# Kernel optimization log

Measured on AMD Instinct MI355X. Metric: run time of the kernel, lower is better.

The kernel has to match this reference:

```python
import jax, jax.numpy as jnp
import numpy as np

K = 1e-3          # sigmoid temperature from MAPLoss(k=0.001): sigmoid(x) = 1/(1+exp(-x/K))
N, D = 512, 128   # batch of embeddings
NUM_CLASSES = 32
EPS = 1e-8


def setup_inputs() -> dict:
    key = jax.random.key(0)
    k1, k2 = jax.random.split(key)
    return {
        "input": jax.random.normal(k1, (N, D), dtype=jnp.float32),
        "target": jax.random.randint(k2, (N,), 0, NUM_CLASSES, dtype=jnp.int64),
    }


def _offdiag_cols(n):
    # cols[i, j] = j-th column index != i, in increasing order (matches
    # torch sm[~eye].view(n, n-1) row-major off-diagonal extraction)
    idx = jnp.arange(n - 1)[None, :]
    rows = jnp.arange(n)[:, None]
    return idx + (idx >= rows)  # [n, n-1] int


def reference(input, target):
    n = input.shape[0]
    # cosine similarity matrix
    norms = jnp.maximum(jnp.linalg.norm(input, axis=1, keepdims=True), EPS)
    xn = input / norms
    sm = xn @ xn.T  # [n, n]

    cols = _offdiag_cols(n)  # [n, n-1]
    ranking = jnp.take_along_axis(sm, cols, axis=1)  # [n, n-1]
    gt_full = (target[None, :] == target[:, None])    # [n, n] bool
    gt = jnp.take_along_axis(gt_full, cols, axis=1).astype(input.dtype)  # [n, n-1]

    # indicator[i, j, l] = sigmoid((r[i, l] - r[i, j]) / K)   -- O(n^3) cube
    indicator = jax.nn.sigmoid((ranking[:, None, :] - ranking[:, :, None]) / K)

    accumulated_gt = jnp.einsum('il,ijl->ij', gt, indicator)  # [n, n-1]
    denom = indicator.sum(-1) + 0.5                           # [n, n-1]
    prec = accumulated_gt / denom
    ap = jnp.sum(gt * prec, axis=1)    # [n]
    num_positives = gt.sum(-1)         # [n]

    valid = num_positives > 0
    ap_norm = jnp.where(valid, ap / jnp.where(valid, num_positives, 1.0), 0.0)
    n_valid = valid.sum().astype(input.dtype)
    return 1.0 - ap_norm.sum() / n_valid
```

## Files before the change

### kernel.cpp

```cpp
#include <hip/hip_runtime.h>

#define N 512
#define D 128
#define TS 32
#define RS_SCALE 1442.6950408889634f
#define W_INV (1.0f / 18.0f)
#define B_OFF 1530.0f
#define PADV -1600.0f
#define NB 172

static __device__ __forceinline__ float rcp_fast(float x) {
    return __builtin_amdgcn_rcpf(x);
}
static __device__ __forceinline__ float exp2_fast(float x) {
    return __builtin_amdgcn_exp2f(x);
}

__global__ __launch_bounds__(256) void map_sim_kernel(
    const float* __restrict__ x, float* __restrict__ rs,
    int* __restrict__ ticket)
{
    const int bi = blockIdx.x, bj = blockIdx.y, t = threadIdx.x;
    __shared__ float As[TS * D], Bs[TS * D];
    __shared__ float ssA[TS], ssB[TS];
    __shared__ float invA[TS], invB[TS];

    if (bi == 0 && bj == 0 && t == 0) *ticket = 0;

    const int lane = t & 63;
#pragma unroll
    for (int r = 0; r < 4; ++r) {
        int ch = t + 256 * r;
        int row = ch >> 5, c4 = ch & 31;
        int sw = (c4 ^ (row >> 1)) << 2;
        float4 va = *(const float4*)(x + (bi * TS + row) * D + c4 * 4);
        *(float4*)(As + row * D + sw) = va;
        float pa = va.x * va.x + va.y * va.y + va.z * va.z + va.w * va.w;
        float4 vb = *(const float4*)(x + (bj * TS + row) * D + c4 * 4);
        *(float4*)(Bs + row * D + sw) = vb;
        float pb = vb.x * vb.x + vb.y * vb.y + vb.z * vb.z + vb.w * vb.w;
#pragma unroll
        for (int off = 16; off; off >>= 1) {
            pa += __shfl_xor(pa, off);
            pb += __shfl_xor(pb, off);
        }
        if ((lane & 31) == 0) { ssA[row] = pa; ssB[row] = pb; }
    }
    __syncthreads();
    if (t < TS)          invA[t] = rcp_fast(fmaxf(sqrtf(ssA[t]), 1e-8f));
    else if (t < 2 * TS) invB[t - TS] = rcp_fast(fmaxf(sqrtf(ssB[t - TS]), 1e-8f));
    __syncthreads();

    const int tx = t & 15, ty = t >> 4;
    float acc00 = 0.f, acc01 = 0.f, acc10 = 0.f, acc11 = 0.f;
#pragma unroll 4
    for (int k4 = 0; k4 < D / 4; ++k4) {
        float4 a0 = *(const float4*)(As + (2 * ty) * D + ((k4 ^ ty) << 2));
        float4 a1 = *(const float4*)(As + (2 * ty + 1) * D + ((k4 ^ ty) << 2));
        float4 b0 = *(const float4*)(Bs + (2 * tx) * D + ((k4 ^ tx) << 2));
        float4 b1 = *(const float4*)(Bs + (2 * tx + 1) * D + ((k4 ^ tx) << 2));
        acc00 = fmaf(a0.x, b0.x, acc00); acc00 = fmaf(a0.y, b0.y, acc00);
        acc00 = fmaf(a0.z, b0.z, acc00); acc00 = fmaf(a0.w, b0.w, acc00);
        acc01 = fmaf(a0.x, b1.x, acc01); acc01 = fmaf(a0.y, b1.y, acc01);
        acc01 = fmaf(a0.z, b1.z, acc01); acc01 = fmaf(a0.w, b1.w, acc01);
        acc10 = fmaf(a1.x, b0.x, acc10); acc10 = fmaf(a1.y, b0.y, acc10);
        acc10 = fmaf(a1.z, b0.z, acc10); acc10 = fmaf(a1.w, b0.w, acc10);
        acc11 = fmaf(a1.x, b1.x, acc11); acc11 = fmaf(a1.y, b1.y, acc11);
        acc11 = fmaf(a1.z, b1.z, acc11); acc11 = fmaf(a1.w, b1.w, acc11);
    }

    const float sA0 = invA[2 * ty] * RS_SCALE;
    const float sA1 = invA[2 * ty + 1] * RS_SCALE;
    const float sB0 = invB[2 * tx], sB1 = invB[2 * tx + 1];
    const int gr = bi * TS + 2 * ty, gc = bj * TS + 2 * tx;
    *(float2*)(rs + gr * N + gc) =
        make_float2(acc00 * sA0 * sB0, acc01 * sA0 * sB1);
    *(float2*)(rs + (gr + 1) * N + gc) =
        make_float2(acc10 * sA1 * sB0, acc11 * sA1 * sB1);
}

__global__ __launch_bounds__(256) void map_ap_kernel(
    const float* __restrict__ rs, const int* __restrict__ tgt,
    float2* __restrict__ av, int* __restrict__ ticket,
    float* __restrict__ out)
{
    const int i = blockIdx.x, t = threadIdx.x;
    const int lane = t & 63;
    __shared__ int hist[256];
    __shared__ int offs[NB];
    __shared__ int wtot[4];
    __shared__ unsigned gbits[16];
    __shared__ __align__(16) float skey[N];
    __shared__ float red[8];
    __shared__ int amLast;

    const int ti = tgt[i];
    const float v0raw = rs[i * N + t];
    const float v1raw = rs[i * N + t + 256];
    const int tg0 = tgt[t], tg1 = tgt[t + 256];

    hist[t] = 0;
    if (t < NB) offs[t] = 0;
    if (t < 16) gbits[t] = 0u;

    float val[2]; int gti[2], q[2];
    val[0] = (t == i) ? PADV : v0raw;
    val[1] = (t + 256 == i) ? PADV : v1raw;
    gti[0] = (t != i && tg0 == ti) ? 1 : 0;
    gti[1] = (t + 256 != i && tg1 == ti) ? 1 : 0;
#pragma unroll
    for (int e = 0; e < 2; ++e) {
        int qq = (int)((val[e] + B_OFF) * W_INV);
        q[e] = max(0, min(NB - 1, qq));
    }
    __syncthreads();
    atomicAdd(&hist[q[0]], (1 << 10) | gti[0]);
    atomicAdd(&hist[q[1]], (1 << 10) | gti[1]);
    __syncthreads();

    int v = hist[t];
#pragma unroll
    for (int off = 1; off < 64; off <<= 1) {
        int u = __shfl_up(v, off);
        if (lane >= off) v += u;
    }
    if (lane == 63) wtot[t >> 6] = v;
    __syncthreads();
    {
        int w = t >> 6, add = 0;
        if (w > 0) add += wtot[0];
        if (w > 1) add += wtot[1];
        if (w > 2) add += wtot[2];
        hist[t] = v + add;
    }
    __syncthreads();

#pragma unroll
    for (int e = 0; e < 2; ++e) {
        int base = (q[e] > 0) ? (hist[q[e] - 1] >> 10) : 0;
        int pos = base + atomicAdd(&offs[q[e]], 1);
        skey[pos] = val[e];
        if (gti[e]) atomicOr(&gbits[pos >> 5], 1u << (pos & 31));
    }
    __syncthreads();

    const int totGt = hist[NB - 1] & 1023;
    const float4* sk4 = (const float4*)skey;

    float apAcc = 0.f, npAcc = 0.f;
#pragma unroll
    for (int ri = 0; ri < 2; ++ri) {
        const int p = t + 256 * ri;
        const float rj = skey[p];
        const float gtj = (float)((gbits[p >> 5] >> (p & 31)) & 1u);
        int qj = (int)((rj + B_OFF) * W_INV);
        qj = max(0, min(NB - 1, qj));
        const int qlo = __shfl(qj, 0);
        const int qhi = __shfl(qj, 63);
        const int lo = (qlo > 1) ? (hist[qlo - 2] >> 10) : 0;
        const int e1 = min(qhi + 1, NB - 1);
        const int hi = hist[e1] >> 10;

        float dsum = (float)(N - hi);
        float gsum = (float)(totGt - (hist[e1] & 1023));

        float d0 = 0.f, d1 = 0.f, d2 = 0.f, d3 = 0.f;
        float g0 = 0.f, g1 = 0.f, g2 = 0.f, g3 = 0.f;
        int k = lo & ~7;
        for (; k + 8 <= hi; k += 8) {
            float4 ka = sk4[k >> 2];
            float4 kb = sk4[(k >> 2) + 1];
            unsigned gw = (gbits[k >> 5] >> (k & 31)) & 0xffu;
            float s0 = rcp_fast(1.f + exp2_fast(rj - ka.x));
            float s1 = rcp_fast(1.f + exp2_fast(rj - ka.y));
            float s2 = rcp_fast(1.f + exp2_fast(rj - ka.z));
            float s3 = rcp_fast(1.f + exp2_fast(rj - ka.w));
            float s4 = rcp_fast(1.f + exp2_fast(rj - kb.x));
            float s5 = rcp_fast(1.f + exp2_fast(rj - kb.y));
            float s6 = rcp_fast(1.f + exp2_fast(rj - kb.z));
            float s7 = rcp_fast(1.f + exp2_fast(rj - kb.w));
            d0 += s0 + s4; d1 += s1 + s5; d2 += s2 + s6; d3 += s3 + s7;
            g0 += ((gw      ) & 1u) ? s0 : 0.f;
            g1 += ((gw >> 1u) & 1u) ? s1 : 0.f;
            g2 += ((gw >> 2u) & 1u) ? s2 : 0.f;
            g3 += ((gw >> 3u) & 1u) ? s3 : 0.f;
            g0 += ((gw >> 4u) & 1u) ? s4 : 0.f;
            g1 += ((gw >> 5u) & 1u) ? s5 : 0.f;
            g2 += ((gw >> 6u) & 1u) ? s6 : 0.f;
            g3 += ((gw >> 7u) & 1u) ? s7 : 0.f;
        }
        dsum += (d0 + d1) + (d2 + d3);
        gsum += (g0 + g1) + (g2 + g3);
        for (; k < hi; ++k) {
            float s = rcp_fast(1.f + exp2_fast(rj - skey[k]));
            dsum += s;
            gsum += ((gbits[k >> 5] >> (k & 31)) & 1u) ? s : 0.f;
        }

        apAcc += gtj * gsum * rcp_fast(dsum + 0.5f);
        npAcc += gtj;
    }

#pragma unroll
    for (int off = 32; off; off >>= 1) {
        apAcc += __shfl_down(apAcc, off);
        npAcc += __shfl_down(npAcc, off);
    }
    if (lane == 0) { red[(t >> 6) * 2] = apAcc; red[(t >> 6) * 2 + 1] = npAcc; }
    __syncthreads();
    if (t == 0) {
        float A = red[0] + red[2] + red[4] + red[6];
        float P = red[1] + red[3] + red[5] + red[7];
        av[i] = make_float2((P > 0.f) ? (A * rcp_fast(P)) : 0.f,
                            (P > 0.f) ? 1.f : 0.f);
        __threadfence();
        int old = atomicAdd(ticket, 1);
        amLast = (old == (int)gridDim.x - 1) ? 1 : 0;
    }
    __syncthreads();

    if (amLast) {
        __threadfence();
        float2 p0 = av[t], p1 = av[t + 256];
        float a = p0.x + p1.x, vv = p0.y + p1.y;
#pragma unroll
        for (int off = 32; off; off >>= 1) {
            a += __shfl_down(a, off);
            vv += __shfl_down(vv, off);
        }
        if (lane == 0) { red[(t >> 6) * 2] = a; red[(t >> 6) * 2 + 1] = vv; }
        __syncthreads();
        if (t == 0) {
            float A = red[0] + red[2] + red[4] + red[6];
            float V = red[1] + red[3] + red[5] + red[7];
            out[0] = 1.0f - A * rcp_fast(V);
        }
    }
}

extern "C" void kernel_launch(void* const* d_in, const int* in_sizes, int n_in,
                              void* d_out, int out_size, void* d_ws, size_t ws_size,
                              hipStream_t stream) {
    const float* x = (const float*)d_in[0];
    const int* tgt = (const int*)d_in[1];
    float* out = (float*)d_out;

    float* rs = (float*)d_ws;
    float2* av = (float2*)((char*)d_ws + N * N * 4);
    int* ticket = (int*)((char*)d_ws + N * N * 4 + N * 8);

    map_sim_kernel<<<dim3(N / TS, N / TS), 256, 0, stream>>>(x, rs, ticket);
    map_ap_kernel<<<N, 256, 0, stream>>>(rs, tgt, av, ticket, out);
}
```

Before: 30.48 us.

## Fuse similarity GEMM into AP kernel with one launch and 512-thread blocks

Drops the separate tiled similarity kernel and the N×N workspace matrix. Each block now computes its own row of cosine similarities directly, reading every row of x from global/L2 and recomputing all row norms per block. Blocks grow to 512 threads, one key per thread, and the ticket counter becomes a modulo-512 rolling counter, so it no longer has to be reset each launch. This removes a kernel launch and the global round trip of the similarity matrix, at the cost of redundant norm and dot work per block and uncoalesced strided row reads.

```diff
diff --git a/kernel.cpp b/kernel.cpp
--- a/kernel.cpp
+++ b/kernel.cpp
@@ -2,7 +2,6 @@
 
 #define N 512
 #define D 128
-#define TS 32
 #define RS_SCALE 1442.6950408889634f
 #define W_INV (1.0f / 18.0f)
 #define B_OFF 1530.0f
@@ -16,117 +15,63 @@
     return __builtin_amdgcn_exp2f(x);
 }
 
-__global__ __launch_bounds__(256) void map_sim_kernel(
-    const float* __restrict__ x, float* __restrict__ rs,
-    int* __restrict__ ticket)
-{
-    const int bi = blockIdx.x, bj = blockIdx.y, t = threadIdx.x;
-    __shared__ float As[TS * D], Bs[TS * D];
-    __shared__ float ssA[TS], ssB[TS];
-    __shared__ float invA[TS], invB[TS];
-
-    if (bi == 0 && bj == 0 && t == 0) *ticket = 0;
-
-    const int lane = t & 63;
-#pragma unroll
-    for (int r = 0; r < 4; ++r) {
-        int ch = t + 256 * r;
-        int row = ch >> 5, c4 = ch & 31;
-        int sw = (c4 ^ (row >> 1)) << 2;
-        float4 va = *(const float4*)(x + (bi * TS + row) * D + c4 * 4);
-        *(float4*)(As + row * D + sw) = va;
-        float pa = va.x * va.x + va.y * va.y + va.z * va.z + va.w * va.w;
-        float4 vb = *(const float4*)(x + (bj * TS + row) * D + c4 * 4);
-        *(float4*)(Bs + row * D + sw) = vb;
-        float pb = vb.x * vb.x + vb.y * vb.y + vb.z * vb.z + vb.w * vb.w;
-#pragma unroll
-        for (int off = 16; off; off >>= 1) {
-            pa += __shfl_xor(pa, off);
-            pb += __shfl_xor(pb, off);
-        }
-        if ((lane & 31) == 0) { ssA[row] = pa; ssB[row] = pb; }
-    }
-    __syncthreads();
-    if (t < TS)          invA[t] = rcp_fast(fmaxf(sqrtf(ssA[t]), 1e-8f));
-    else if (t < 2 * TS) invB[t - TS] = rcp_fast(fmaxf(sqrtf(ssB[t - TS]), 1e-8f));
-    __syncthreads();
-
-    const int tx = t & 15, ty = t >> 4;
-    float acc00 = 0.f, acc01 = 0.f, acc10 = 0.f, acc11 = 0.f;
-#pragma unroll 4
-    for (int k4 = 0; k4 < D / 4; ++k4) {
-        float4 a0 = *(const float4*)(As + (2 * ty) * D + ((k4 ^ ty) << 2));
-        float4 a1 = *(const float4*)(As + (2 * ty + 1) * D + ((k4 ^ ty) << 2));
-        float4 b0 = *(const float4*)(Bs + (2 * tx) * D + ((k4 ^ tx) << 2));
-        float4 b1 = *(const float4*)(Bs + (2 * tx + 1) * D + ((k4 ^ tx) << 2));
-        acc00 = fmaf(a0.x, b0.x, acc00); acc00 = fmaf(a0.y, b0.y, acc00);
-        acc00 = fmaf(a0.z, b0.z, acc00); acc00 = fmaf(a0.w, b0.w, acc00);
-        acc01 = fmaf(a0.x, b1.x, acc01); acc01 = fmaf(a0.y, b1.y, acc01);
-        acc01 = fmaf(a0.z, b1.z, acc01); acc01 = fmaf(a0.w, b1.w, acc01);
-        acc10 = fmaf(a1.x, b0.x, acc10); acc10 = fmaf(a1.y, b0.y, acc10);
-        acc10 = fmaf(a1.z, b0.z, acc10); acc10 = fmaf(a1.w, b0.w, acc10);
-        acc11 = fmaf(a1.x, b1.x, acc11); acc11 = fmaf(a1.y, b1.y, acc11);
-        acc11 = fmaf(a1.z, b1.z, acc11); acc11 = fmaf(a1.w, b1.w, acc11);
-    }
-
-    const float sA0 = invA[2 * ty] * RS_SCALE;
-    const float sA1 = invA[2 * ty + 1] * RS_SCALE;
-    const float sB0 = invB[2 * tx], sB1 = invB[2 * tx + 1];
-    const int gr = bi * TS + 2 * ty, gc = bj * TS + 2 * tx;
-    *(float2*)(rs + gr * N + gc) =
-        make_float2(acc00 * sA0 * sB0, acc01 * sA0 * sB1);
-    *(float2*)(rs + (gr + 1) * N + gc) =
-        make_float2(acc10 * sA1 * sB0, acc11 * sA1 * sB1);
-}
-
-__global__ __launch_bounds__(256) void map_ap_kernel(
-    const float* __restrict__ rs, const int* __restrict__ tgt,
-    float2* __restrict__ av, int* __restrict__ ticket,
+__global__ __launch_bounds__(512) void map_all_kernel(
+    const float* __restrict__ x, const int* __restrict__ tgt,
+    float2* __restrict__ av, unsigned* __restrict__ ticket,
     float* __restrict__ out)
 {
     const int i = blockIdx.x, t = threadIdx.x;
     const int lane = t & 63;
+    __shared__ __align__(16) float xi[D];
+    __shared__ float sInvI;
     __shared__ int hist[256];
     __shared__ int offs[NB];
     __shared__ int wtot[4];
     __shared__ unsigned gbits[16];
     __shared__ __align__(16) float skey[N];
-    __shared__ float red[8];
+    __shared__ float red[16];
     __shared__ int amLast;
 
-    const int ti = tgt[i];
-    const float v0raw = rs[i * N + t];
-    const float v1raw = rs[i * N + t + 256];
-    const int tg0 = tgt[t], tg1 = tgt[t + 256];
-
-    hist[t] = 0;
+    if (t < D) xi[t] = x[i * D + t];
+    if (t < 256) hist[t] = 0;
     if (t < NB) offs[t] = 0;
     if (t < 16) gbits[t] = 0u;
-
-    float val[2]; int gti[2], q[2];
-    val[0] = (t == i) ? PADV : v0raw;
-    val[1] = (t + 256 == i) ? PADV : v1raw;
-    gti[0] = (t != i && tg0 == ti) ? 1 : 0;
-    gti[1] = (t + 256 != i && tg1 == ti) ? 1 : 0;
-#pragma unroll
-    for (int e = 0; e < 2; ++e) {
-        int qq = (int)((val[e] + B_OFF) * W_INV);
-        q[e] = max(0, min(NB - 1, qq));
-    }
-    __syncthreads();
-    atomicAdd(&hist[q[0]], (1 << 10) | gti[0]);
-    atomicAdd(&hist[q[1]], (1 << 10) | gti[1]);
     __syncthreads();
 
-    int v = hist[t];
+    const float4* xc = (const float4*)(x + t * D);
+    const float4* xi4 = (const float4*)xi;
+    float dot = 0.f, ss = 0.f;
+#pragma unroll 8
+    for (int k = 0; k < D / 4; ++k) {
+        float4 v = xc[k];
+        float4 u = xi4[k];
+        dot = fmaf(v.x, u.x, dot); dot = fmaf(v.y, u.y, dot);
+        dot = fmaf(v.z, u.z, dot); dot = fmaf(v.w, u.w, dot);
+        ss = fmaf(v.x, v.x, ss); ss = fmaf(v.y, v.y, ss);
+        ss = fmaf(v.z, v.z, ss); ss = fmaf(v.w, v.w, ss);
+    }
+    const float invT = rcp_fast(fmaxf(sqrtf(ss), 1e-8f));
+    if (t == i) sInvI = invT;
+    __syncthreads();
+
+    const int ti = tgt[i];
+    const bool self = (t == i);
+    const float val = self ? PADV : dot * invT * sInvI * RS_SCALE;
+    const int gti = (!self && tgt[t] == ti) ? 1 : 0;
+    int q = (int)((val + B_OFF) * W_INV);
+    q = max(0, min(NB - 1, q));
+    atomicAdd(&hist[q], (1 << 10) | gti);
+    __syncthreads();
+
+    int v = (t < 256) ? hist[t] : 0;
 #pragma unroll
     for (int off = 1; off < 64; off <<= 1) {
         int u = __shfl_up(v, off);
         if (lane >= off) v += u;
     }
-    if (lane == 63) wtot[t >> 6] = v;
+    if (t < 256 && lane == 63) wtot[t >> 6] = v;
     __syncthreads();
-    {
+    if (t < 256) {
         int w = t >> 6, add = 0;
         if (w > 0) add += wtot[0];
         if (w > 1) add += wtot[1];
@@ -135,71 +80,65 @@
     }
     __syncthreads();
 
-#pragma unroll
-    for (int e = 0; e < 2; ++e) {
-        int base = (q[e] > 0) ? (hist[q[e] - 1] >> 10) : 0;
-        int pos = base + atomicAdd(&offs[q[e]], 1);
-        skey[pos] = val[e];
-        if (gti[e]) atomicOr(&gbits[pos >> 5], 1u << (pos & 31));
+    {
+        int base = (q > 0) ? (hist[q - 1] >> 10) : 0;
+        int pos = base + atomicAdd(&offs[q], 1);
+        skey[pos] = val;
+        if (gti) atomicOr(&gbits[pos >> 5], 1u << (pos & 31));
     }
     __syncthreads();
 
     const int totGt = hist[NB - 1] & 1023;
     const float4* sk4 = (const float4*)skey;
 
-    float apAcc = 0.f, npAcc = 0.f;
-#pragma unroll
-    for (int ri = 0; ri < 2; ++ri) {
-        const int p = t + 256 * ri;
-        const float rj = skey[p];
-        const float gtj = (float)((gbits[p >> 5] >> (p & 31)) & 1u);
-        int qj = (int)((rj + B_OFF) * W_INV);
-        qj = max(0, min(NB - 1, qj));
-        const int qlo = __shfl(qj, 0);
-        const int qhi = __shfl(qj, 63);
-        const int lo = (qlo > 1) ? (hist[qlo - 2] >> 10) : 0;
-        const int e1 = min(qhi + 1, NB - 1);
-        const int hi = hist[e1] >> 10;
+    const float rj = skey[t];
+    const float gtj = (float)((gbits[t >> 5] >> (t & 31)) & 1u);
+    int qj = (int)((rj + B_OFF) * W_INV);
+    qj = max(0, min(NB - 1, qj));
+    const int qlo = __shfl(qj, 0);
+    const int qhi = __shfl(qj, 63);
+    const int lo = (qlo > 1) ? (hist[qlo - 2] >> 10) : 0;
+    const int e1 = min(qhi + 1, NB - 1);
+    const int hi = hist[e1] >> 10;
 
-        float dsum = (float)(N - hi);
-        float gsum = (float)(totGt - (hist[e1] & 1023));
+    float dsum = (float)(N - hi);
+    float gsum = (float)(totGt - (hist[e1] & 1023));
 
-        float d0 = 0.f, d1 = 0.f, d2 = 0.f, d3 = 0.f;
-        float g0 = 0.f, g1 = 0.f, g2 = 0.f, g3 = 0.f;
-        int k = lo & ~7;
-        for (; k + 8 <= hi; k += 8) {
-            float4 ka = sk4[k >> 2];
-            float4 kb = sk4[(k >> 2) + 1];
-            unsigned gw = (gbits[k >> 5] >> (k & 31)) & 0xffu;
-            float s0 = rcp_fast(1.f + exp2_fast(rj - ka.x));
-            float s1 = rcp_fast(1.f + exp2_fast(rj - ka.y));
-            float s2 = rcp_fast(1.f + exp2_fast(rj - ka.z));
-            float s3 = rcp_fast(1.f + exp2_fast(rj - ka.w));
-            float s4 = rcp_fast(1.f + exp2_fast(rj - kb.x));
-            float s5 = rcp_fast(1.f + exp2_fast(rj - kb.y));
-            float s6 = rcp_fast(1.f + exp2_fast(rj - kb.z));
-            float s7 = rcp_fast(1.f + exp2_fast(rj - kb.w));
-            d0 += s0 + s4; d1 += s1 + s5; d2 += s2 + s6; d3 += s3 + s7;
-            g0 += ((gw      ) & 1u) ? s0 : 0.f;
-            g1 += ((gw >> 1u) & 1u) ? s1 : 0.f;
-            g2 += ((gw >> 2u) & 1u) ? s2 : 0.f;
-            g3 += ((gw >> 3u) & 1u) ? s3 : 0.f;
-            g0 += ((gw >> 4u) & 1u) ? s4 : 0.f;
-            g1 += ((gw >> 5u) & 1u) ? s5 : 0.f;
-            g2 += ((gw >> 6u) & 1u) ? s6 : 0.f;
-            g3 += ((gw >> 7u) & 1u) ? s7 : 0.f;
-        }
-        dsum += (d0 + d1) + (d2 + d3);
-        gsum += (g0 + g1) + (g2 + g3);
-        for (; k < hi; ++k) {
-            float s = rcp_fast(1.f + exp2_fast(rj - skey[k]));
-            dsum += s;
-            gsum += ((gbits[k >> 5] >> (k & 31)) & 1u) ? s : 0.f;
-        }
+    float d0 = 0.f, d1 = 0.f, d2 = 0.f, d3 = 0.f;
+    float g0 = 0.f, g1 = 0.f, g2 = 0.f, g3 = 0.f;
+    int k = lo & ~7;
+    for (; k + 8 <= hi; k += 8) {
+        float4 ka = sk4[k >> 2];
+        float4 kb = sk4[(k >> 2) + 1];
+        unsigned gw = (gbits[k >> 5] >> (k & 31)) & 0xffu;
+        float s0 = rcp_fast(1.f + exp2_fast(rj - ka.x));
+        float s1 = rcp_fast(1.f + exp2_fast(rj - ka.y));
+        float s2 = rcp_fast(1.f + exp2_fast(rj - ka.z));
+        float s3 = rcp_fast(1.f + exp2_fast(rj - ka.w));
+        float s4 = rcp_fast(1.f + exp2_fast(rj - kb.x));
+        float s5 = rcp_fast(1.f + exp2_fast(rj - kb.y));
+        float s6 = rcp_fast(1.f + exp2_fast(rj - kb.z));
+        float s7 = rcp_fast(1.f + exp2_fast(rj - kb.w));
+        d0 += s0 + s4; d1 += s1 + s5; d2 += s2 + s6; d3 += s3 + s7;
+        g0 += ((gw      ) & 1u) ? s0 : 0.f;
+        g1 += ((gw >> 1u) & 1u) ? s1 : 0.f;
+        g2 += ((gw >> 2u) & 1u) ? s2 : 0.f;
+        g3 += ((gw >> 3u) & 1u) ? s3 : 0.f;
+        g0 += ((gw >> 4u) & 1u) ? s4 : 0.f;
+        g1 += ((gw >> 5u) & 1u) ? s5 : 0.f;
+        g2 += ((gw >> 6u) & 1u) ? s6 : 0.f;
+        g3 += ((gw >> 7u) & 1u) ? s7 : 0.f;
+    }
+    dsum += (d0 + d1) + (d2 + d3);
+    gsum += (g0 + g1) + (g2 + g3);
+    for (; k < hi; ++k) {
+        float s = rcp_fast(1.f + exp2_fast(rj - skey[k]));
+        dsum += s;
+        gsum += ((gbits[k >> 5] >> (k & 31)) & 1u) ? s : 0.f;
+    }
 
-        apAcc += gtj * gsum * rcp_fast(dsum + 0.5f);
-        npAcc += gtj;
-    }
+    float apAcc = gtj * gsum * rcp_fast(dsum + 0.5f);
+    float npAcc = gtj;
 
 #pragma unroll
     for (int off = 32; off; off >>= 1) {
@@ -209,20 +148,21 @@
     if (lane == 0) { red[(t >> 6) * 2] = apAcc; red[(t >> 6) * 2 + 1] = npAcc; }
     __syncthreads();
     if (t == 0) {
-        float A = red[0] + red[2] + red[4] + red[6];
-        float P = red[1] + red[3] + red[5] + red[7];
+        float A = 0.f, P = 0.f;
+#pragma unroll
+        for (int kk = 0; kk < 8; ++kk) { A += red[2 * kk]; P += red[2 * kk + 1]; }
         av[i] = make_float2((P > 0.f) ? (A * rcp_fast(P)) : 0.f,
                             (P > 0.f) ? 1.f : 0.f);
         __threadfence();
-        int old = atomicAdd(ticket, 1);
-        amLast = (old == (int)gridDim.x - 1) ? 1 : 0;
+        unsigned old = atomicAdd(ticket, 1u);
+        amLast = ((old & 511u) == 511u) ? 1 : 0;
     }
     __syncthreads();
 
     if (amLast) {
         __threadfence();
-        float2 p0 = av[t], p1 = av[t + 256];
-        float a = p0.x + p1.x, vv = p0.y + p1.y;
+        float2 p = av[t];
+        float a = p.x, vv = p.y;
 #pragma unroll
         for (int off = 32; off; off >>= 1) {
             a += __shfl_down(a, off);
@@ -231,8 +171,9 @@
         if (lane == 0) { red[(t >> 6) * 2] = a; red[(t >> 6) * 2 + 1] = vv; }
         __syncthreads();
         if (t == 0) {
-            float A = red[0] + red[2] + red[4] + red[6];
-            float V = red[1] + red[3] + red[5] + red[7];
+            float A = 0.f, V = 0.f;
+#pragma unroll
+            for (int kk = 0; kk < 8; ++kk) { A += red[2 * kk]; V += red[2 * kk + 1]; }
             out[0] = 1.0f - A * rcp_fast(V);
         }
     }
@@ -245,10 +186,8 @@
     const int* tgt = (const int*)d_in[1];
     float* out = (float*)d_out;
 
-    float* rs = (float*)d_ws;
-    float2* av = (float2*)((char*)d_ws + N * N * 4);
-    int* ticket = (int*)((char*)d_ws + N * N * 4 + N * 8);
+    float2* av = (float2*)d_ws;
+    unsigned* ticket = (unsigned*)((char*)d_ws + 4096);
 
-    map_sim_kernel<<<dim3(N / TS, N / TS), 256, 0, stream>>>(x, rs, ticket);
-    map_ap_kernel<<<N, 256, 0, stream>>>(rs, tgt, av, ticket, out);
+    map_all_kernel<<<N, 512, 0, stream>>>(x, tgt, av, ticket, out);
 }
```

Result: slower. 36.43 us (+19.5%).
